# Optimization experiments

Hardware: AMD Instinct MI355X
Metric: run time of the kernel (lower is better)

The kernel has to match this reference:

```python
import jax, jax.numpy as jnp
import numpy as np

B, T, D_IN, D_OUT = 4, 4096, 1024, 64


def setup_inputs() -> dict:
    key = jax.random.key(0)
    k_x, k_q, k_k, k_v = jax.random.split(key, 4)
    scale = 1.0 / np.sqrt(D_IN)  # ~nn.Linear init scale
    return {
        "x": jax.random.normal(k_x, (B, T, D_IN), dtype=jnp.float32),
        "Wq": jax.random.normal(k_q, (D_IN, D_OUT), dtype=jnp.float32) * scale,
        "Wk": jax.random.normal(k_k, (D_IN, D_OUT), dtype=jnp.float32) * scale,
        "Wv": jax.random.normal(k_v, (D_IN, D_OUT), dtype=jnp.float32) * scale,
    }


def reference(x, Wq, Wk, Wv):
    # x: [B, T, D_in]; W*: [D_in, D_out]
    Q = jnp.einsum("btd,de->bte", x, Wq)
    K = jnp.einsum("btd,de->bte", x, Wk)
    V = jnp.einsum("btd,de->bte", x, Wv)
    n_tokens = x.shape[1]
    dk = 1.0 / jnp.sqrt(jnp.asarray(Q.shape[-1], dtype=Q.dtype))
    # scores: [B, T, T]
    scores = jnp.einsum("bqe,bke->bqk", Q, K) * dk
    # causal mask: -inf above the diagonal (triu with diagonal=1)
    causal = jnp.tril(jnp.ones((n_tokens, n_tokens), dtype=bool))
    scores = jnp.where(causal[None, :, :], scores, -jnp.inf)
    attn = jax.nn.softmax(scores, axis=-1)
    # dropout=0.0 (eval / deterministic reference)
    out = jnp.einsum("bqk,bke->bqe", attn, V)
    return out
```

## Files before the change

### kernel.cpp

```cpp
#include <hip/hip_runtime.h>

typedef unsigned short u16;
typedef __bf16 bf16x8 __attribute__((ext_vector_type(8)));
typedef float f32x4 __attribute__((ext_vector_type(4)));
typedef unsigned short u16x4 __attribute__((ext_vector_type(4)));
typedef unsigned short u16x8 __attribute__((ext_vector_type(8)));

#define T_SEQ 4096
#define DIN 1024
#define DH 64
#define NSPLIT 4

static __device__ __forceinline__ u16 f2bf(float f) {
    return __builtin_bit_cast(u16, (__bf16)f);
}

__global__ __launch_bounds__(256) void transpose_w(
    const float* __restrict__ Wq, const float* __restrict__ Wk,
    const float* __restrict__ Wv, u16* __restrict__ Wt)
{
    int idx = blockIdx.x * 256 + threadIdx.x;
    int m   = idx >> 12;
    int rem = idx & 4095;
    int e   = rem & 63;
    int k0  = (rem >> 6) << 4;
    const float* W = (m == 0) ? Wq : (m == 1 ? Wk : Wv);
    u16x8 v0, v1;
#pragma unroll
    for (int i = 0; i < 8; i++) v0[i] = f2bf(W[(size_t)(k0 + i) * DH + e]);
#pragma unroll
    for (int i = 0; i < 8; i++) v1[i] = f2bf(W[(size_t)(k0 + 8 + i) * DH + e]);
    u16* dst = Wt + ((size_t)m * DH + e) * DIN + k0;
    *(u16x8*)(dst)     = v0;
    *(u16x8*)(dst + 8) = v1;
}

__global__ __launch_bounds__(512, 4) void qkv_proj(
    const float* __restrict__ x, const u16* __restrict__ Wt,
    u16* __restrict__ Qb, u16* __restrict__ Kb, u16* __restrict__ Vtg)
{
    const int r0   = blockIdx.x * 32;
    const int tid  = threadIdx.x;
    const int w    = tid >> 6;
    const int wm   = w >> 2;
    const int wn   = w & 3;
    const int lane = tid & 63;
    const int lg   = lane >> 4, li = lane & 15;

    __shared__ union {
        struct {
            u16 xs[2][32][72];
            u16 ws[2][192][72];
        } s;
        u16 epi[32][200];
    } lds;

    const int xrow = tid >> 4;
    const int xoff = (tid & 15) * 4;
    const float* xp = x + (size_t)(r0 + xrow) * DIN + xoff;

    f32x4 acc[3];
#pragma unroll
    for (int nr = 0; nr < 3; nr++) acc[nr] = (f32x4){0.f, 0.f, 0.f, 0.f};

    {
        float4 a = *(const float4*)(xp);
        u16x4 xa;
        xa[0] = f2bf(a.x); xa[1] = f2bf(a.y); xa[2] = f2bf(a.z); xa[3] = f2bf(a.w);
        *(u16x4*)&lds.s.xs[0][xrow][xoff] = xa;
#pragma unroll
        for (int j = 0; j < 3; j++) {
            int c = tid + 512 * j;
            int wr = c >> 3, wo = (c & 7) * 8;
            u16x8 wv = *(const u16x8*)(Wt + (size_t)wr * DIN + wo);
            *(u16x8*)&lds.s.ws[0][wr][wo] = wv;
        }
    }
    __syncthreads();

    int cur = 0;
#pragma unroll 1
    for (int ks = 0; ks < 16; ++ks) {
        const bool have_next = ks < 15;
        const int k0n = (ks + 1) * 64;

        float4 na;
        u16x8 nw[3];
        if (have_next) {
            na = *(const float4*)(xp + k0n);
#pragma unroll
            for (int j = 0; j < 3; j++) {
                int c = tid + 512 * j;
                nw[j] = *(const u16x8*)(Wt + (size_t)(c >> 3) * DIN + k0n + (c & 7) * 8);
            }
        }

        bf16x8 af0 = *(const bf16x8*)&lds.s.xs[cur][wm * 16 + li][lg * 8];
        bf16x8 af1 = *(const bf16x8*)&lds.s.xs[cur][wm * 16 + li][32 + lg * 8];
#pragma unroll
        for (int nr = 0; nr < 3; nr++) {
            bf16x8 b0 = *(const bf16x8*)&lds.s.ws[cur][wn * 48 + nr * 16 + li][lg * 8];
            bf16x8 b1 = *(const bf16x8*)&lds.s.ws[cur][wn * 48 + nr * 16 + li][32 + lg * 8];
            acc[nr] = __builtin_amdgcn_mfma_f32_16x16x32_bf16(af0, b0, acc[nr], 0, 0, 0);
            acc[nr] = __builtin_amdgcn_mfma_f32_16x16x32_bf16(af1, b1, acc[nr], 0, 0, 0);
        }

        if (have_next) {
            u16x4 xa;
            xa[0] = f2bf(na.x); xa[1] = f2bf(na.y); xa[2] = f2bf(na.z); xa[3] = f2bf(na.w);
            *(u16x4*)&lds.s.xs[cur ^ 1][xrow][xoff] = xa;
#pragma unroll
            for (int j = 0; j < 3; j++) {
                int c = tid + 512 * j;
                *(u16x8*)&lds.s.ws[cur ^ 1][c >> 3][(c & 7) * 8] = nw[j];
            }
        }
        __syncthreads();
        cur ^= 1;
    }

#pragma unroll
    for (int nr = 0; nr < 3; nr++)
#pragma unroll
        for (int rr = 0; rr < 4; rr++)
            lds.epi[wm * 16 + lg * 4 + rr][wn * 48 + nr * 16 + li] = f2bf(acc[nr][rr]);
    __syncthreads();

    {
        const int row = tid >> 4;
        const int c0  = (tid & 15) * 8;
        u16x8 v = *(const u16x8*)&lds.epi[row][c0];
        u16* dst = (c0 < 64) ? (Qb + (size_t)(r0 + row) * DH + c0)
                             : (Kb + (size_t)(r0 + row) * DH + (c0 - 64));
        *(u16x8*)dst = v;
    }
    {
        const int e  = tid & 63;
        const int g  = tid >> 6;
        const int bb = r0 >> 12;
        const int tb = r0 & 4095;
        u16x4 ov;
#pragma unroll
        for (int j = 0; j < 4; j++) ov[j] = lds.epi[g * 4 + j][128 + e];
        *(u16x4*)(Vtg + ((size_t)bb * DH + e) * T_SEQ + tb + g * 4) = ov;
    }
}

__global__ __launch_bounds__(256) void flash_attn(
    const u16* __restrict__ Qb, const u16* __restrict__ Kb,
    const u16* __restrict__ Vtg, float* __restrict__ opart,
    float* __restrict__ lpart)
{
    const int bid  = blockIdx.x;
    const int sp   = bid & (NSPLIT - 1);
    const int qt   = 63 - ((bid >> 2) & 63);
    const int b    = bid >> 8;
    const int tid  = threadIdx.x;
    const int w    = tid >> 6;
    const int lane = tid & 63;
    const int lg   = lane >> 4, li = lane & 15;

    const int q0 = qt * 64 + w * 16;

    const u16* Qp = Qb + ((size_t)b * T_SEQ + q0) * DH;
    const u16* Kp = Kb + (size_t)b * T_SEQ * DH;
    const u16* Vp = Vtg + (size_t)b * DH * T_SEQ;

    __shared__ u16 kbuf[2][64][72];
    __shared__ u16 vbuf[2][80][72];
    __shared__ u16 p_lds[4][16][72];
    u16 (*pl)[72] = p_lds[w];

    const int srow = tid >> 2;
    const int scol = (tid & 3) * 16;

    {
        const u16 one = f2bf(1.0f);
        for (int i = tid; i < 16 * 72; i += 256) {
            int r = i / 72, c = i - r * 72;
            u16 v = (r == 0) ? one : (u16)0;
            vbuf[0][64 + r][c] = v;
            vbuf[1][64 + r][c] = v;
        }
    }

    bf16x8 qf0 = *(const bf16x8*)(Qp + (size_t)li * DH + lg * 8);
    bf16x8 qf1 = *(const bf16x8*)(Qp + (size_t)li * DH + 32 + lg * 8);

    f32x4 o[5];
#pragma unroll
    for (int t = 0; t < 5; t++) o[t] = (f32x4){0.f, 0.f, 0.f, 0.f};

    const float c_sc = 0.125f * 1.44269504f;

    if (sp <= qt) {
        const int kv0 = sp * 64;
        u16x8 k0 = *(const u16x8*)(Kp + (size_t)(kv0 + srow) * DH + scol);
        u16x8 k1 = *(const u16x8*)(Kp + (size_t)(kv0 + srow) * DH + scol + 8);
        u16x8 v0 = *(const u16x8*)(Vp + (size_t)srow * T_SEQ + kv0 + scol);
        u16x8 v1 = *(const u16x8*)(Vp + (size_t)srow * T_SEQ + kv0 + scol + 8);
        *(u16x8*)&kbuf[0][srow][scol]     = k0;
        *(u16x8*)&kbuf[0][srow][scol + 8] = k1;
        *(u16x8*)&vbuf[0][srow][scol]     = v0;
        *(u16x8*)&vbuf[0][srow][scol + 8] = v1;
    }
    __syncthreads();

    int cur = 0;
    for (int kt = sp; kt <= qt; kt += NSPLIT) {
        const bool have_next = (kt + NSPLIT) <= qt;
        u16x8 nk0, nk1, nv0, nv1;
        if (have_next) {
            const int kv1 = (kt + NSPLIT) * 64;
            nk0 = *(const u16x8*)(Kp + (size_t)(kv1 + srow) * DH + scol);
            nk1 = *(const u16x8*)(Kp + (size_t)(kv1 + srow) * DH + scol + 8);
            nv0 = *(const u16x8*)(Vp + (size_t)srow * T_SEQ + kv1 + scol);
            nv1 = *(const u16x8*)(Vp + (size_t)srow * T_SEQ + kv1 + scol + 8);
        }

        f32x4 s[4];
#pragma unroll
        for (int t = 0; t < 4; t++) s[t] = (f32x4){0.f, 0.f, 0.f, 0.f};
#pragma unroll
        for (int t = 0; t < 4; t++) {
            bf16x8 kc0 = *(const bf16x8*)&kbuf[cur][t * 16 + li][lg * 8];
            bf16x8 kc1 = *(const bf16x8*)&kbuf[cur][t * 16 + li][32 + lg * 8];
            s[t] = __builtin_amdgcn_mfma_f32_16x16x32_bf16(qf0, kc0, s[t], 0, 0, 0);
            s[t] = __builtin_amdgcn_mfma_f32_16x16x32_bf16(qf1, kc1, s[t], 0, 0, 0);
        }

        if (kt == qt) {
#pragma unroll
            for (int t = 0; t < 4; t++)
#pragma unroll
                for (int r = 0; r < 4; r++) {
                    int qrow = w * 16 + lg * 4 + r;
                    int kcol = t * 16 + li;
                    float p = (kcol > qrow) ? 0.f
                              : __builtin_amdgcn_exp2f(s[t][r] * c_sc);
                    pl[lg * 4 + r][t * 16 + li] = f2bf(p);
                }
        } else {
#pragma unroll
            for (int t = 0; t < 4; t++)
#pragma unroll
                for (int r = 0; r < 4; r++)
                    pl[lg * 4 + r][t * 16 + li] =
                        f2bf(__builtin_amdgcn_exp2f(s[t][r] * c_sc));
        }

        bf16x8 pa0 = *(const bf16x8*)(&pl[li][lg * 8]);
        bf16x8 pa1 = *(const bf16x8*)(&pl[li][32 + lg * 8]);

#pragma unroll
        for (int t = 0; t < 5; t++) {
            bf16x8 vc0 = *(const bf16x8*)&vbuf[cur][t * 16 + li][lg * 8];
            bf16x8 vc1 = *(const bf16x8*)&vbuf[cur][t * 16 + li][32 + lg * 8];
            o[t] = __builtin_amdgcn_mfma_f32_16x16x32_bf16(pa0, vc0, o[t], 0, 0, 0);
            o[t] = __builtin_amdgcn_mfma_f32_16x16x32_bf16(pa1, vc1, o[t], 0, 0, 0);
        }

        if (have_next) {
            *(u16x8*)&kbuf[cur ^ 1][srow][scol]     = nk0;
            *(u16x8*)&kbuf[cur ^ 1][srow][scol + 8] = nk1;
            *(u16x8*)&vbuf[cur ^ 1][srow][scol]     = nv0;
            *(u16x8*)&vbuf[cur ^ 1][srow][scol + 8] = nv1;
        }
        __syncthreads();
        cur ^= 1;
    }

    const int p = (b * 64 + qt) * NSPLIT + sp;
    float* op = opart + (size_t)p * 64 * 64;
#pragma unroll
    for (int t = 0; t < 4; t++)
#pragma unroll
        for (int r = 0; r < 4; r++) {
            int row = w * 16 + lg * 4 + r;
            op[(size_t)row * 64 + t * 16 + li] = o[t][r];
        }
    if (li == 0) {
#pragma unroll
        for (int r = 0; r < 4; r++) {
            int row = w * 16 + lg * 4 + r;
            lpart[(size_t)p * 64 + row] = o[4][r];
        }
    }
}

__global__ __launch_bounds__(64) void attn_combine(
    const float* __restrict__ opart, const float* __restrict__ lpart,
    float* __restrict__ out)
{
    const int bid = blockIdx.x;
    const int rg  = bid & 3;
    const int qt  = (bid >> 2) & 63;
    const int b   = bid >> 8;
    const int pb  = (b * 64 + qt) * NSPLIT;
    const int row = rg * 16 + (threadIdx.x >> 2);
    const int c0  = (threadIdx.x & 3) * 16;

    float den = 0.f;
#pragma unroll
    for (int s = 0; s < NSPLIT; s++) den += lpart[(size_t)(pb + s) * 64 + row];

    float4 acc[4];
#pragma unroll
    for (int j = 0; j < 4; j++) acc[j] = (float4){0.f, 0.f, 0.f, 0.f};
#pragma unroll
    for (int s = 0; s < NSPLIT; s++) {
        const float* op = opart + ((size_t)(pb + s) * 64 + row) * 64 + c0;
#pragma unroll
        for (int j = 0; j < 4; j++) {
            float4 v = *(const float4*)(op + j * 4);
            acc[j].x += v.x; acc[j].y += v.y;
            acc[j].z += v.z; acc[j].w += v.w;
        }
    }
    float inv = 1.f / den;
    float* dst = out + ((size_t)(b * T_SEQ + qt * 64 + row)) * DH + c0;
#pragma unroll
    for (int j = 0; j < 4; j++) {
        float4 v = {acc[j].x * inv, acc[j].y * inv, acc[j].z * inv, acc[j].w * inv};
        *(float4*)(dst + j * 4) = v;
    }
}

extern "C" void kernel_launch(void* const* d_in, const int* in_sizes, int n_in,
                              void* d_out, int out_size, void* d_ws, size_t ws_size,
                              hipStream_t stream) {
    const float* x  = (const float*)d_in[0];
    const float* Wq = (const float*)d_in[1];
    const float* Wk = (const float*)d_in[2];
    const float* Wv = (const float*)d_in[3];
    float* out = (float*)d_out;

    char* ws = (char*)d_ws;
    u16*   Wt    = (u16*)(ws);
    u16*   Qb    = (u16*)(ws + 393216);
    u16*   Kb    = (u16*)(ws + 2490368);
    u16*   Vt    = (u16*)(ws + 4587520);
    float* opart = (float*)(ws + 6684672);
    float* lpart = (float*)(ws + 23461888);

    hipLaunchKernelGGL(transpose_w,  dim3(48),   dim3(256), 0, stream, Wq, Wk, Wv, Wt);
    hipLaunchKernelGGL(qkv_proj,     dim3(512),  dim3(512), 0, stream, x, Wt, Qb, Kb, Vt);
    hipLaunchKernelGGL(flash_attn,   dim3(1024), dim3(256), 0, stream, Qb, Kb, Vt, opart, lpart);
    hipLaunchKernelGGL(attn_combine, dim3(1024), dim3(64),  0, stream, opart, lpart, out);
}
```

Measured before the change: 147.3 us.

## Enlarge flash-attention query tile to 128 rows and compute row sums in registers

Each flash_attn block now handles 128 query rows, 32 per wave, instead of 64. Every K/V tile loaded into LDS is therefore reused by twice as many queries, and the grid is halved to 512 blocks. The softmax denominator was previously obtained by appending a ones row to the V buffer and running an extra MFMA; it is now accumulated in registers and reduced with lane shuffles. Waves skip KV tiles beyond their own causal diagonal. The trade-offs are higher register pressure, fewer blocks to spread across CUs, and more load imbalance between waves.

```diff
diff --git a/kernel.cpp b/kernel.cpp
--- a/kernel.cpp
+++ b/kernel.cpp
@@ -146,54 +146,58 @@
     }
 }
 
-__global__ __launch_bounds__(256) void flash_attn(
+__global__ __launch_bounds__(256, 2) void flash_attn(
     const u16* __restrict__ Qb, const u16* __restrict__ Kb,
     const u16* __restrict__ Vtg, float* __restrict__ opart,
     float* __restrict__ lpart)
 {
     const int bid  = blockIdx.x;
     const int sp   = bid & (NSPLIT - 1);
-    const int qt   = 63 - ((bid >> 2) & 63);
-    const int b    = bid >> 8;
+    const int qt   = 31 - ((bid >> 2) & 31);
+    const int b    = bid >> 7;
     const int tid  = threadIdx.x;
     const int w    = tid >> 6;
     const int lane = tid & 63;
     const int lg   = lane >> 4, li = lane & 15;
 
-    const int q0 = qt * 64 + w * 16;
-
-    const u16* Qp = Qb + ((size_t)b * T_SEQ + q0) * DH;
+    const int q0 = qt * 128;
+    const int qw = q0 + w * 32;
+
+    const u16* Qp = Qb + ((size_t)b * T_SEQ + qw) * DH;
     const u16* Kp = Kb + (size_t)b * T_SEQ * DH;
     const u16* Vp = Vtg + (size_t)b * DH * T_SEQ;
 
     __shared__ u16 kbuf[2][64][72];
-    __shared__ u16 vbuf[2][80][72];
-    __shared__ u16 p_lds[4][16][72];
+    __shared__ u16 vbuf[2][64][72];
+    __shared__ u16 p_lds[4][32][72];
     u16 (*pl)[72] = p_lds[w];
 
     const int srow = tid >> 2;
     const int scol = (tid & 3) * 16;
 
-    {
-        const u16 one = f2bf(1.0f);
-        for (int i = tid; i < 16 * 72; i += 256) {
-            int r = i / 72, c = i - r * 72;
-            u16 v = (r == 0) ? one : (u16)0;
-            vbuf[0][64 + r][c] = v;
-            vbuf[1][64 + r][c] = v;
-        }
-    }
-
-    bf16x8 qf0 = *(const bf16x8*)(Qp + (size_t)li * DH + lg * 8);
-    bf16x8 qf1 = *(const bf16x8*)(Qp + (size_t)li * DH + 32 + lg * 8);
-
-    f32x4 o[5];
-#pragma unroll
-    for (int t = 0; t < 5; t++) o[t] = (f32x4){0.f, 0.f, 0.f, 0.f};
+    bf16x8 qf[2][2];
+#pragma unroll
+    for (int h = 0; h < 2; h++) {
+        qf[h][0] = *(const bf16x8*)(Qp + (size_t)(h * 16 + li) * DH + lg * 8);
+        qf[h][1] = *(const bf16x8*)(Qp + (size_t)(h * 16 + li) * DH + 32 + lg * 8);
+    }
+
+    f32x4 o[2][4];
+#pragma unroll
+    for (int h = 0; h < 2; h++)
+#pragma unroll
+        for (int t = 0; t < 4; t++) o[h][t] = (f32x4){0.f, 0.f, 0.f, 0.f};
+    float rs[2][4];
+#pragma unroll
+    for (int h = 0; h < 2; h++)
+#pragma unroll
+        for (int r = 0; r < 4; r++) rs[h][r] = 0.f;
 
     const float c_sc = 0.125f * 1.44269504f;
-
-    if (sp <= qt) {
+    const int ktmax = 2 * qt + 1;
+    const int ktd   = 2 * qt + (w >> 1);
+
+    if (sp <= ktmax) {
         const int kv0 = sp * 64;
         u16x8 k0 = *(const u16x8*)(Kp + (size_t)(kv0 + srow) * DH + scol);
         u16x8 k1 = *(const u16x8*)(Kp + (size_t)(kv0 + srow) * DH + scol + 8);
@@ -207,8 +211,8 @@
     __syncthreads();
 
     int cur = 0;
-    for (int kt = sp; kt <= qt; kt += NSPLIT) {
-        const bool have_next = (kt + NSPLIT) <= qt;
+    for (int kt = sp; kt <= ktmax; kt += NSPLIT) {
+        const bool have_next = (kt + NSPLIT) <= ktmax;
         u16x8 nk0, nk1, nv0, nv1;
         if (have_next) {
             const int kv1 = (kt + NSPLIT) * 64;
@@ -218,46 +222,65 @@
             nv1 = *(const u16x8*)(Vp + (size_t)srow * T_SEQ + kv1 + scol + 8);
         }
 
-        f32x4 s[4];
-#pragma unroll
-        for (int t = 0; t < 4; t++) s[t] = (f32x4){0.f, 0.f, 0.f, 0.f};
-#pragma unroll
-        for (int t = 0; t < 4; t++) {
-            bf16x8 kc0 = *(const bf16x8*)&kbuf[cur][t * 16 + li][lg * 8];
-            bf16x8 kc1 = *(const bf16x8*)&kbuf[cur][t * 16 + li][32 + lg * 8];
-            s[t] = __builtin_amdgcn_mfma_f32_16x16x32_bf16(qf0, kc0, s[t], 0, 0, 0);
-            s[t] = __builtin_amdgcn_mfma_f32_16x16x32_bf16(qf1, kc1, s[t], 0, 0, 0);
-        }
-
-        if (kt == qt) {
-#pragma unroll
-            for (int t = 0; t < 4; t++)
-#pragma unroll
-                for (int r = 0; r < 4; r++) {
-                    int qrow = w * 16 + lg * 4 + r;
-                    int kcol = t * 16 + li;
-                    float p = (kcol > qrow) ? 0.f
-                              : __builtin_amdgcn_exp2f(s[t][r] * c_sc);
-                    pl[lg * 4 + r][t * 16 + li] = f2bf(p);
-                }
-        } else {
-#pragma unroll
-            for (int t = 0; t < 4; t++)
-#pragma unroll
-                for (int r = 0; r < 4; r++)
-                    pl[lg * 4 + r][t * 16 + li] =
-                        f2bf(__builtin_amdgcn_exp2f(s[t][r] * c_sc));
-        }
-
-        bf16x8 pa0 = *(const bf16x8*)(&pl[li][lg * 8]);
-        bf16x8 pa1 = *(const bf16x8*)(&pl[li][32 + lg * 8]);
-
-#pragma unroll
-        for (int t = 0; t < 5; t++) {
-            bf16x8 vc0 = *(const bf16x8*)&vbuf[cur][t * 16 + li][lg * 8];
-            bf16x8 vc1 = *(const bf16x8*)&vbuf[cur][t * 16 + li][32 + lg * 8];
-            o[t] = __builtin_amdgcn_mfma_f32_16x16x32_bf16(pa0, vc0, o[t], 0, 0, 0);
-            o[t] = __builtin_amdgcn_mfma_f32_16x16x32_bf16(pa1, vc1, o[t], 0, 0, 0);
+        if (kt <= ktd) {
+            f32x4 s[2][4];
+#pragma unroll
+            for (int h = 0; h < 2; h++)
+#pragma unroll
+                for (int t = 0; t < 4; t++) s[h][t] = (f32x4){0.f, 0.f, 0.f, 0.f};
+#pragma unroll
+            for (int t = 0; t < 4; t++) {
+                bf16x8 kc0 = *(const bf16x8*)&kbuf[cur][t * 16 + li][lg * 8];
+                bf16x8 kc1 = *(const bf16x8*)&kbuf[cur][t * 16 + li][32 + lg * 8];
+                s[0][t] = __builtin_amdgcn_mfma_f32_16x16x32_bf16(qf[0][0], kc0, s[0][t], 0, 0, 0);
+                s[0][t] = __builtin_amdgcn_mfma_f32_16x16x32_bf16(qf[0][1], kc1, s[0][t], 0, 0, 0);
+                s[1][t] = __builtin_amdgcn_mfma_f32_16x16x32_bf16(qf[1][0], kc0, s[1][t], 0, 0, 0);
+                s[1][t] = __builtin_amdgcn_mfma_f32_16x16x32_bf16(qf[1][1], kc1, s[1][t], 0, 0, 0);
+            }
+
+            const int kv0 = kt * 64;
+            if (kt == ktd) {
+#pragma unroll
+                for (int h = 0; h < 2; h++)
+#pragma unroll
+                    for (int t = 0; t < 4; t++)
+#pragma unroll
+                        for (int r = 0; r < 4; r++) {
+                            int qrow = qw + h * 16 + lg * 4 + r;
+                            int kcol = kv0 + t * 16 + li;
+                            float p = (kcol > qrow) ? 0.f
+                                      : __builtin_amdgcn_exp2f(s[h][t][r] * c_sc);
+                            rs[h][r] += p;
+                            pl[h * 16 + lg * 4 + r][t * 16 + li] = f2bf(p);
+                        }
+            } else {
+#pragma unroll
+                for (int h = 0; h < 2; h++)
+#pragma unroll
+                    for (int t = 0; t < 4; t++)
+#pragma unroll
+                        for (int r = 0; r < 4; r++) {
+                            float p = __builtin_amdgcn_exp2f(s[h][t][r] * c_sc);
+                            rs[h][r] += p;
+                            pl[h * 16 + lg * 4 + r][t * 16 + li] = f2bf(p);
+                        }
+            }
+
+            bf16x8 pa[2][2];
+#pragma unroll
+            for (int h = 0; h < 2; h++) {
+                pa[h][0] = *(const bf16x8*)(&pl[h * 16 + li][lg * 8]);
+                pa[h][1] = *(const bf16x8*)(&pl[h * 16 + li][32 + lg * 8]);
+            }
+#pragma unroll
+            for (int t = 0; t < 4; t++) {
+                bf16x8 vc0 = *(const bf16x8*)&vbuf[cur][t * 16 + li][lg * 8];
+                bf16x8 vc1 = *(const bf16x8*)&vbuf[cur][t * 16 + li][32 + lg * 8];
+                o[0][t] = __builtin_amdgcn_mfma_f32_16x16x32_bf16(pa[0][0], vc0, o[0][t], 0, 0, 0);
+                o[0][t] = __builtin_amdgcn_mfma_f32_16x16x32_bf16(pa[0][1], vc1, o[0][t], 0, 0, 0);
+                o[1][t] = __builtin_amdgcn_mfma_f32_16x16x32_bf16(pa[1][0], vc0, o[1][t], 0, 0, 0);
+                o[1][t] = __builtin_amdgcn_mfma_f32_16x16x32_bf16(pa[1][1], vc1, o[1][t], 0, 0, 0);
+            }
         }
 
         if (have_next) {
@@ -270,22 +293,31 @@
         cur ^= 1;
     }
 
-    const int p = (b * 64 + qt) * NSPLIT + sp;
-    float* op = opart + (size_t)p * 64 * 64;
-#pragma unroll
-    for (int t = 0; t < 4; t++)
+    const int p = (b * 32 + qt) * NSPLIT + sp;
+    float* op = opart + (size_t)p * 128 * 64;
+#pragma unroll
+    for (int h = 0; h < 2; h++)
+#pragma unroll
+        for (int t = 0; t < 4; t++)
+#pragma unroll
+            for (int r = 0; r < 4; r++) {
+                int row = w * 32 + h * 16 + lg * 4 + r;
+                op[(size_t)row * 64 + t * 16 + li] = o[h][t][r];
+            }
+#pragma unroll
+    for (int h = 0; h < 2; h++)
 #pragma unroll
         for (int r = 0; r < 4; r++) {
-            int row = w * 16 + lg * 4 + r;
-            op[(size_t)row * 64 + t * 16 + li] = o[t][r];
-        }
-    if (li == 0) {
-#pragma unroll
-        for (int r = 0; r < 4; r++) {
-            int row = w * 16 + lg * 4 + r;
-            lpart[(size_t)p * 64 + row] = o[4][r];
-        }
-    }
+            float v = rs[h][r];
+            v += __shfl_xor(v, 1);
+            v += __shfl_xor(v, 2);
+            v += __shfl_xor(v, 4);
+            v += __shfl_xor(v, 8);
+            if (li == 0) {
+                int row = w * 32 + h * 16 + lg * 4 + r;
+                lpart[(size_t)p * 128 + row] = v;
+            }
+        }
 }
 
 __global__ __launch_bounds__(64) void attn_combine(
@@ -293,23 +325,23 @@
     float* __restrict__ out)
 {
     const int bid = blockIdx.x;
-    const int rg  = bid & 3;
-    const int qt  = (bid >> 2) & 63;
+    const int rg  = bid & 7;
+    const int qt  = (bid >> 3) & 31;
     const int b   = bid >> 8;
-    const int pb  = (b * 64 + qt) * NSPLIT;
+    const int pb  = (b * 32 + qt) * NSPLIT;
     const int row = rg * 16 + (threadIdx.x >> 2);
     const int c0  = (threadIdx.x & 3) * 16;
 
     float den = 0.f;
 #pragma unroll
-    for (int s = 0; s < NSPLIT; s++) den += lpart[(size_t)(pb + s) * 64 + row];
+    for (int s = 0; s < NSPLIT; s++) den += lpart[(size_t)(pb + s) * 128 + row];
 
     float4 acc[4];
 #pragma unroll
     for (int j = 0; j < 4; j++) acc[j] = (float4){0.f, 0.f, 0.f, 0.f};
 #pragma unroll
     for (int s = 0; s < NSPLIT; s++) {
-        const float* op = opart + ((size_t)(pb + s) * 64 + row) * 64 + c0;
+        const float* op = opart + ((size_t)(pb + s) * 128 + row) * 64 + c0;
 #pragma unroll
         for (int j = 0; j < 4; j++) {
             float4 v = *(const float4*)(op + j * 4);
@@ -318,7 +350,7 @@
         }
     }
     float inv = 1.f / den;
-    float* dst = out + ((size_t)(b * T_SEQ + qt * 64 + row)) * DH + c0;
+    float* dst = out + ((size_t)(b * T_SEQ + qt * 128 + row)) * DH + c0;
 #pragma unroll
     for (int j = 0; j < 4; j++) {
         float4 v = {acc[j].x * inv, acc[j].y * inv, acc[j].z * inv, acc[j].w * inv};
@@ -345,6 +377,6 @@
 
     hipLaunchKernelGGL(transpose_w,  dim3(48),   dim3(256), 0, stream, Wq, Wk, Wv, Wt);
     hipLaunchKernelGGL(qkv_proj,     dim3(512),  dim3(512), 0, stream, x, Wt, Qb, Kb, Vt);
-    hipLaunchKernelGGL(flash_attn,   dim3(1024), dim3(256), 0, stream, Qb, Kb, Vt, opart, lpart);
+    hipLaunchKernelGGL(flash_attn,   dim3(512),  dim3(256), 0, stream, Qb, Kb, Vt, opart, lpart);
     hipLaunchKernelGGL(attn_combine, dim3(1024), dim3(64),  0, stream, opart, lpart, out);
 }
```

New measurement: 151.0 us. 1.02x slower.
